# Performance work log

Hardware: AMD Instinct MI355X
Metric: run time of the kernel (lower is better)

Reference implementation:

```python
import jax, jax.numpy as jnp
import numpy as np

D_MODEL = 1024
N_EXPERTS = 8
TOP_K = 2
BOTTLENECK = 64
B, S = 2, 4096
ADAPTER_SCALE = 0.5


def setup_inputs() -> dict:
    key = jax.random.key(0)
    ks = jax.random.split(key, 8)
    sd = 0.02
    x = jax.random.normal(ks[0], (B, S, D_MODEL), dtype=jnp.float32)
    w_gate = jax.random.normal(ks[1], (D_MODEL, N_EXPERTS), dtype=jnp.float32) * sd
    w_noise = jax.random.normal(ks[2], (D_MODEL, N_EXPERTS), dtype=jnp.float32) * sd
    Wd = jax.random.normal(ks[3], (N_EXPERTS, D_MODEL, BOTTLENECK), dtype=jnp.float32) * sd
    bd = jnp.zeros((N_EXPERTS, BOTTLENECK), dtype=jnp.float32)
    Wu = jax.random.normal(ks[4], (N_EXPERTS, BOTTLENECK, D_MODEL), dtype=jnp.float32) * sd
    bu = jnp.zeros((N_EXPERTS, D_MODEL), dtype=jnp.float32)
    return {"x": x, "w_gate": w_gate, "w_noise": w_noise,
            "Wd": Wd, "bd": bd, "Wu": Wu, "bu": bu}


def _moe_forward(x, w_gate, w_noise, Wd, bd, Wu, bu):
    b, s, d = x.shape
    xf = x.reshape(-1, d)                      # [T, D] flattened tokens
    T = xf.shape[0]

    # --- noisy top-k gating (eval mode: no noise added, logits = clean) ---
    clean_logits = xf @ w_gate                 # [T, E]
    logits = clean_logits
    k1 = min(TOP_K + 1, N_EXPERTS)
    top_logits, top_idx = jax.lax.top_k(logits, k1)
    top_k_logits = top_logits[:, :TOP_K]       # [T, k]
    top_k_idx = top_idx[:, :TOP_K]             # [T, k]
    top_k_gates = jax.nn.softmax(top_k_logits, axis=-1)
    rows = jnp.arange(T)[:, None]
    gates = jnp.zeros((T, N_EXPERTS), dtype=top_k_gates.dtype)
    gates = gates.at[rows, top_k_idx].set(top_k_gates)  # sparse gate matrix [T, E]

    # --- experts (AdaptFormer adapters): dense compute, sparse combine ---
    # mathematically identical to SparseDispatcher dispatch/combine:
    # out[t] = sum_e gates[t,e] * expert_e(x[t])  (gates zero off top-k)
    h = jax.nn.relu(jnp.einsum('td,edb->teb', xf, Wd) + bd[None, :, :])  # [T,E,b]
    y = jnp.einsum('teb,ebd->ted', h, Wu) + bu[None, :, :]               # [T,E,D]
    y = ADAPTER_SCALE * y
    out = jnp.einsum('te,ted->td', gates, y)   # weighted combine (index_add equiv)
    return out.reshape(b, s, d)


def reference(x, w_gate, w_noise, Wd, bd, Wu, bu):
    return _moe_forward(x, w_gate, w_noise, Wd, bd, Wu, bu)
```

## Files before the change

kernel.cpp:

```cpp
#include <hip/hip_runtime.h>
#include <stdint.h>

#define T_TOK 8192
#define DM    1024
#define NE    8
#define BOT   64
#define HD    512
#define HD2   576
#define PW    8

typedef __attribute__((ext_vector_type(8))) short bf16x8;
typedef __attribute__((ext_vector_type(4))) short bf16x4;
typedef __attribute__((ext_vector_type(4))) float f32x4;

__device__ __forceinline__ ushort f2bf(float f) {
  union { float f; uint32_t u; } v; v.f = f;
  uint32_t r = (v.u + 0x7fffu + ((v.u >> 16) & 1u)) >> 16;
  return (ushort)r;
}

__global__ __launch_bounds__(256, 2)
void prep_kernel(const float* __restrict__ x, const float* __restrict__ wg,
                 ushort* __restrict__ Xb, float* __restrict__ sg,
                 ushort* __restrict__ H2) {
  __shared__ float part[4][PW][NE];
  __shared__ float sgl[PW][NE];
  const int lane = threadIdx.x & 63;
  const int w    = threadIdx.x >> 6;
  const int t0   = blockIdx.x * PW;
  const int dd   = w * 256 + lane * 4;

  float4 wgr[4][2];
  #pragma unroll
  for (int j = 0; j < 4; ++j) {
    wgr[j][0] = *(const float4*)(wg + (size_t)(dd + j) * NE);
    wgr[j][1] = *(const float4*)(wg + (size_t)(dd + j) * NE + 4);
  }
  const int ebit = ((lane & 1) << 2) | (lane & 2) | ((lane >> 2) & 1);

  const float* xp = x + (size_t)t0 * DM + dd;
  float4 xv = *(const float4*)xp;
  #pragma unroll
  for (int tk = 0; tk < PW; ++tk) {
    float4 nxt = {};
    if (tk + 1 < PW) nxt = *(const float4*)(xp + (size_t)(tk + 1) * DM);
    bf16x4 xb;
    xb[0] = (short)f2bf(xv.x); xb[1] = (short)f2bf(xv.y);
    xb[2] = (short)f2bf(xv.z); xb[3] = (short)f2bf(xv.w);
    *(bf16x4*)(Xb + (size_t)(t0 + tk) * DM + dd) = xb;
    float a[NE] = {};
    const float* xs = (const float*)&xv;
    #pragma unroll
    for (int j = 0; j < 4; ++j) {
      const float xj = xs[j];
      const float* wr = (const float*)&wgr[j][0];
      #pragma unroll
      for (int e = 0; e < NE; ++e) a[e] += xj * wr[e];
    }
    float t0v[4];
    #pragma unroll
    for (int j = 0; j < 4; ++j) {
      float send = (lane & 1) ? a[j] : a[j + 4];
      float keep = (lane & 1) ? a[j + 4] : a[j];
      t0v[j] = keep + __shfl_xor(send, 1);
    }
    float t1v[2];
    #pragma unroll
    for (int j = 0; j < 2; ++j) {
      float send = (lane & 2) ? t0v[j] : t0v[j + 2];
      float keep = (lane & 2) ? t0v[j + 2] : t0v[j];
      t1v[j] = keep + __shfl_xor(send, 2);
    }
    {
      float send = (lane & 4) ? t1v[0] : t1v[1];
      float keep = (lane & 4) ? t1v[1] : t1v[0];
      float t2 = keep + __shfl_xor(send, 4);
      t2 += __shfl_xor(t2, 8);
      t2 += __shfl_xor(t2, 16);
      t2 += __shfl_xor(t2, 32);
      if (lane < NE) part[w][tk][ebit] = t2;
    }
    xv = nxt;
  }
  __syncthreads();

  const int tid = threadIdx.x;
  if (tid < PW) {
    float lg[NE];
    #pragma unroll
    for (int e = 0; e < NE; ++e)
      lg[e] = part[0][tid][e] + part[1][tid][e] + part[2][tid][e] + part[3][tid][e];
    int e0 = 0; float l0 = lg[0];
    #pragma unroll
    for (int e = 1; e < NE; ++e) if (lg[e] > l0) { l0 = lg[e]; e0 = e; }
    int e1 = -1; float l1 = -3.4e38f;
    #pragma unroll
    for (int e = 0; e < NE; ++e) if (e != e0 && lg[e] > l1) { l1 = lg[e]; e1 = e; }
    const float p1  = __expf(l1 - l0);
    const float inv = 1.f / (1.f + p1);
    const float g0 = 0.5f * inv, g1 = 0.5f * p1 * inv;
    float g[NE];
    #pragma unroll
    for (int e = 0; e < NE; ++e) g[e] = (e == e0) ? g0 : ((e == e1) ? g1 : 0.f);
    #pragma unroll
    for (int e = 0; e < NE; ++e) sgl[tid][e] = g[e];
    *(float4*)(sg + (size_t)(t0 + tid) * NE)     = *(float4*)&g[0];
    *(float4*)(sg + (size_t)(t0 + tid) * NE + 4) = *(float4*)&g[4];
  }
  __syncthreads();

  if (tid < PW * 8) {
    const int tk = tid >> 3, ch = tid & 7;
    bf16x8 v;
    #pragma unroll
    for (int k = 0; k < 8; ++k)
      v[k] = (ch == 0) ? (short)f2bf(sgl[tk][k]) : (short)0;
    *(bf16x8*)(H2 + (size_t)(t0 + tk) * HD2 + HD + ch * 8) = v;
  }
}

__global__ __launch_bounds__(256)
void cvt_w_kernel(const float* __restrict__ Wd, const float* __restrict__ Wu,
                  const float* __restrict__ bu,
                  ushort* __restrict__ WdT, ushort* __restrict__ Wu2T) {
  __shared__ ushort tl[64][72];
  const int rr = threadIdx.x >> 2;
  const int cc = (threadIdx.x & 3) * 16;
  const int bx = blockIdx.x;
  if (bx < 128) {
    const int e  = bx >> 4;
    const int d0 = (bx & 15) * 64;
    const float* src = Wd + ((size_t)e * DM + d0 + rr) * BOT + cc;
    #pragma unroll
    for (int i = 0; i < 4; ++i) {
      float4 v = *(const float4*)(src + i * 4);
      tl[rr][cc + i * 4 + 0] = f2bf(v.x);
      tl[rr][cc + i * 4 + 1] = f2bf(v.y);
      tl[rr][cc + i * 4 + 2] = f2bf(v.z);
      tl[rr][cc + i * 4 + 3] = f2bf(v.w);
    }
    __syncthreads();
    bf16x8 o0, o1;
    #pragma unroll
    for (int k = 0; k < 8; ++k) o0[k] = (short)tl[cc + k][rr];
    #pragma unroll
    for (int k = 0; k < 8; ++k) o1[k] = (short)tl[cc + 8 + k][rr];
    ushort* dst = WdT + ((size_t)e * BOT + rr) * DM + d0 + cc;
    *(bf16x8*)dst       = o0;
    *(bf16x8*)(dst + 8) = o1;
  } else {
    const int b2 = bx - 128;
    const int n0 = (b2 >> 4) * 64;
    const int d0 = (b2 & 15) * 64;
    const int n  = n0 + rr;
    #pragma unroll
    for (int i = 0; i < 4; ++i) {
      float4 v;
      if (n < HD)           v = *(const float4*)(Wu + (size_t)n * DM + d0 + cc + i * 4);
      else if (n < HD + NE) v = *(const float4*)(bu + (size_t)(n - HD) * DM + d0 + cc + i * 4);
      else { v.x = 0.f; v.y = 0.f; v.z = 0.f; v.w = 0.f; }
      tl[rr][cc + i * 4 + 0] = f2bf(v.x);
      tl[rr][cc + i * 4 + 1] = f2bf(v.y);
      tl[rr][cc + i * 4 + 2] = f2bf(v.z);
      tl[rr][cc + i * 4 + 3] = f2bf(v.w);
    }
    __syncthreads();
    bf16x8 o0, o1;
    #pragma unroll
    for (int k = 0; k < 8; ++k) o0[k] = (short)tl[cc + k][rr];
    #pragma unroll
    for (int k = 0; k < 8; ++k) o1[k] = (short)tl[cc + 8 + k][rr];
    ushort* dst = Wu2T + (size_t)(d0 + rr) * HD2 + n0 + cc;
    *(bf16x8*)dst       = o0;
    *(bf16x8*)(dst + 8) = o1;
  }
}

template <int EPI, int NKT, int NBX>
__global__ __launch_bounds__(256)
void gemm_bt(const ushort* __restrict__ A, const ushort* __restrict__ B,
             const float* __restrict__ sg, const float* __restrict__ bd,
             ushort* __restrict__ Hout, float* __restrict__ Cout, int nwg) {
  constexpr int K = NKT * 64;
  __shared__ __attribute__((aligned(16))) ushort sA[2][128 * 64];
  __shared__ __attribute__((aligned(16))) ushort sB[2][128 * 64];
  const int lane = threadIdx.x & 63;
  const int w    = threadIdx.x >> 6;
  const int lb = (blockIdx.x % 8) * (nwg / 8) + blockIdx.x / 8;
  const int tile_m = (lb / NBX) * 128;
  const int tile_n = (lb % NBX) * 128;
  const int wm = (w >> 1) * 64;
  const int wn = (w & 1) * 64;
  const int sr = lane >> 3;
  const int sc = ((lane & 7) * 8) ^ (sr << 3);
  const int lr = lane & 15;
  const int kg = lane >> 4;
  const int swz = (lr & 7) << 3;
  f32x4 acc[4][4] = {};

#define STAGE(buf, kt) do {                                                       \
    const int k0_ = (kt) << 6;                                                    \
    _Pragma("unroll")                                                             \
    for (int c = 0; c < 4; ++c) {                                                 \
      const ushort* ga = A + (size_t)(tile_m + w * 32 + c * 8 + sr) * K + k0_ + sc; \
      __builtin_amdgcn_global_load_lds((const __attribute__((address_space(1))) void*)ga, \
          (__attribute__((address_space(3))) void*)&sA[buf][(w * 32 + c * 8) * 64], 16, 0, 0); \
      const ushort* gb = B + (size_t)(tile_n + w * 32 + c * 8 + sr) * K + k0_ + sc; \
      __builtin_amdgcn_global_load_lds((const __attribute__((address_space(1))) void*)gb, \
          (__attribute__((address_space(3))) void*)&sB[buf][(w * 32 + c * 8) * 64], 16, 0, 0); \
    } } while (0)

  STAGE(0, 0);
  for (int kt = 0; kt < NKT; ++kt) {
    const int cur = kt & 1;
    if (kt + 1 < NKT) {
      STAGE(cur ^ 1, kt + 1);
      asm volatile("s_waitcnt vmcnt(8)" ::: "memory");
    } else {
      asm volatile("s_waitcnt vmcnt(0)" ::: "memory");
    }
    __builtin_amdgcn_s_barrier();
    #pragma unroll
    for (int s = 0; s < 2; ++s) {
      bf16x8 af[4], bfr[4];
      #pragma unroll
      for (int i = 0; i < 4; ++i)
        af[i] = *(const bf16x8*)&sA[cur][(wm + i * 16 + lr) * 64 + ((s * 32 + kg * 8) ^ swz)];
      #pragma unroll
      for (int j = 0; j < 4; ++j)
        bfr[j] = *(const bf16x8*)&sB[cur][(wn + j * 16 + lr) * 64 + ((s * 32 + kg * 8) ^ swz)];
      #pragma unroll
      for (int i = 0; i < 4; ++i)
        #pragma unroll
        for (int j = 0; j < 4; ++j)
          acc[i][j] = __builtin_amdgcn_mfma_f32_16x16x32_bf16(af[i], bfr[j], acc[i][j], 0, 0, 0);
    }
    asm volatile("" ::: "memory");
    __builtin_amdgcn_s_barrier();
  }
#undef STAGE

  if (EPI == 0) {
    const int e = (tile_n + wn) >> 6;
    float bdv[4];
    #pragma unroll
    for (int j = 0; j < 4; ++j) bdv[j] = bd[tile_n + wn + j * 16 + lr];
    #pragma unroll
    for (int i = 0; i < 4; ++i) {
      #pragma unroll
      for (int r = 0; r < 4; ++r) {
        const int t = tile_m + wm + i * 16 + kg * 4 + r;
        const float sglv = sg[(size_t)t * NE + e];
        #pragma unroll
        for (int j = 0; j < 4; ++j) {
          float v = fmaxf(acc[i][j][r] + bdv[j], 0.f) * sglv;
          Hout[(size_t)t * HD2 + tile_n + wn + j * 16 + lr] = f2bf(v);
        }
      }
    }
  } else {
    #pragma unroll
    for (int i = 0; i < 4; ++i) {
      #pragma unroll
      for (int r = 0; r < 4; ++r) {
        const int t = tile_m + wm + i * 16 + kg * 4 + r;
        #pragma unroll
        for (int j = 0; j < 4; ++j)
          Cout[(size_t)t * DM + tile_n + wn + j * 16 + lr] = acc[i][j][r];
      }
    }
  }
}

extern "C" void kernel_launch(void* const* d_in, const int* in_sizes, int n_in,
                              void* d_out, int out_size, void* d_ws, size_t ws_size,
                              hipStream_t stream) {
  const float* x  = (const float*)d_in[0];
  const float* wg = (const float*)d_in[1];
  const float* Wd = (const float*)d_in[3];
  const float* bd = (const float*)d_in[4];
  const float* Wu = (const float*)d_in[5];
  const float* bu = (const float*)d_in[6];
  float* out = (float*)d_out;

  char* ws = (char*)d_ws;
  ushort* Xb   = (ushort*)(ws);
  ushort* H2   = (ushort*)(ws + 16777216);
  ushort* WdT  = (ushort*)(ws + 26214400);
  ushort* Wu2T = (ushort*)(ws + 27262976);
  float*  sgw  = (float*) (ws + 28442624);

  prep_kernel <<<dim3(T_TOK / PW), dim3(256), 0, stream>>>(x, wg, Xb, sgw, H2);
  cvt_w_kernel<<<dim3(272),        dim3(256), 0, stream>>>(Wd, Wu, bu, WdT, Wu2T);

  gemm_bt<0, 16, 4><<<dim3(256), dim3(256), 0, stream>>>(Xb, WdT, sgw, bd, H2, nullptr, 256);
  gemm_bt<1, 9, 8><<<dim3(512), dim3(256), 0, stream>>>(H2, Wu2T, sgw, nullptr, nullptr, out, 512);
}
```

Before: 55.54 us.

## Merge prep and weight-convert kernels, use 128x64 GEMM tiles with triple buffering

Merges the token prep/gating kernel and the weight conversion kernel into a single launch, with blocks selected by block index, to save one launch and let the two jobs overlap. The GEMM tile shrinks from 128x128 to 128x64, doubling the grid to 512 and 1024 workgroups for better CU coverage. The shared-memory pipeline goes from double to triple buffering with two tiles prefetched ahead, waitcnts adjusted to match. Smaller N tiles reload more of A per output and lower MFMA work per LDS read.

After: 50.38 us. 1.1x faster.

```diff
diff --git a/kernel.cpp b/kernel.cpp
--- a/kernel.cpp
+++ b/kernel.cpp
@@ -8,6 +8,7 @@
 #define HD    512
 #define HD2   576
 #define PW    8
+#define NPREP (T_TOK / PW)
 
 typedef __attribute__((ext_vector_type(8))) short bf16x8;
 typedef __attribute__((ext_vector_type(4))) short bf16x4;
@@ -20,159 +21,155 @@
 }
 
 __global__ __launch_bounds__(256, 2)
-void prep_kernel(const float* __restrict__ x, const float* __restrict__ wg,
-                 ushort* __restrict__ Xb, float* __restrict__ sg,
-                 ushort* __restrict__ H2) {
+void prep_cvt_kernel(const float* __restrict__ x, const float* __restrict__ wg,
+                     const float* __restrict__ Wd, const float* __restrict__ Wu,
+                     const float* __restrict__ bu,
+                     ushort* __restrict__ Xb, float* __restrict__ sg,
+                     ushort* __restrict__ H2, ushort* __restrict__ WdT,
+                     ushort* __restrict__ Wu2T) {
   __shared__ float part[4][PW][NE];
   __shared__ float sgl[PW][NE];
-  const int lane = threadIdx.x & 63;
-  const int w    = threadIdx.x >> 6;
-  const int t0   = blockIdx.x * PW;
-  const int dd   = w * 256 + lane * 4;
-
-  float4 wgr[4][2];
-  #pragma unroll
-  for (int j = 0; j < 4; ++j) {
-    wgr[j][0] = *(const float4*)(wg + (size_t)(dd + j) * NE);
-    wgr[j][1] = *(const float4*)(wg + (size_t)(dd + j) * NE + 4);
-  }
-  const int ebit = ((lane & 1) << 2) | (lane & 2) | ((lane >> 2) & 1);
-
-  const float* xp = x + (size_t)t0 * DM + dd;
-  float4 xv = *(const float4*)xp;
-  #pragma unroll
-  for (int tk = 0; tk < PW; ++tk) {
-    float4 nxt = {};
-    if (tk + 1 < PW) nxt = *(const float4*)(xp + (size_t)(tk + 1) * DM);
-    bf16x4 xb;
-    xb[0] = (short)f2bf(xv.x); xb[1] = (short)f2bf(xv.y);
-    xb[2] = (short)f2bf(xv.z); xb[3] = (short)f2bf(xv.w);
-    *(bf16x4*)(Xb + (size_t)(t0 + tk) * DM + dd) = xb;
-    float a[NE] = {};
-    const float* xs = (const float*)&xv;
+  __shared__ ushort tl[64][72];
+  if (blockIdx.x < NPREP) {
+    const int lane = threadIdx.x & 63;
+    const int w    = threadIdx.x >> 6;
+    const int t0   = blockIdx.x * PW;
+    const int dd   = w * 256 + lane * 4;
+    float4 wgr[4][2];
     #pragma unroll
     for (int j = 0; j < 4; ++j) {
-      const float xj = xs[j];
-      const float* wr = (const float*)&wgr[j][0];
-      #pragma unroll
-      for (int e = 0; e < NE; ++e) a[e] += xj * wr[e];
-    }
-    float t0v[4];
-    #pragma unroll
-    for (int j = 0; j < 4; ++j) {
-      float send = (lane & 1) ? a[j] : a[j + 4];
-      float keep = (lane & 1) ? a[j + 4] : a[j];
-      t0v[j] = keep + __shfl_xor(send, 1);
-    }
-    float t1v[2];
-    #pragma unroll
-    for (int j = 0; j < 2; ++j) {
-      float send = (lane & 2) ? t0v[j] : t0v[j + 2];
-      float keep = (lane & 2) ? t0v[j + 2] : t0v[j];
-      t1v[j] = keep + __shfl_xor(send, 2);
-    }
-    {
-      float send = (lane & 4) ? t1v[0] : t1v[1];
-      float keep = (lane & 4) ? t1v[1] : t1v[0];
-      float t2 = keep + __shfl_xor(send, 4);
-      t2 += __shfl_xor(t2, 8);
-      t2 += __shfl_xor(t2, 16);
-      t2 += __shfl_xor(t2, 32);
-      if (lane < NE) part[w][tk][ebit] = t2;
-    }
-    xv = nxt;
-  }
-  __syncthreads();
-
-  const int tid = threadIdx.x;
-  if (tid < PW) {
-    float lg[NE];
-    #pragma unroll
-    for (int e = 0; e < NE; ++e)
-      lg[e] = part[0][tid][e] + part[1][tid][e] + part[2][tid][e] + part[3][tid][e];
-    int e0 = 0; float l0 = lg[0];
-    #pragma unroll
-    for (int e = 1; e < NE; ++e) if (lg[e] > l0) { l0 = lg[e]; e0 = e; }
-    int e1 = -1; float l1 = -3.4e38f;
-    #pragma unroll
-    for (int e = 0; e < NE; ++e) if (e != e0 && lg[e] > l1) { l1 = lg[e]; e1 = e; }
-    const float p1  = __expf(l1 - l0);
-    const float inv = 1.f / (1.f + p1);
-    const float g0 = 0.5f * inv, g1 = 0.5f * p1 * inv;
-    float g[NE];
-    #pragma unroll
-    for (int e = 0; e < NE; ++e) g[e] = (e == e0) ? g0 : ((e == e1) ? g1 : 0.f);
-    #pragma unroll
-    for (int e = 0; e < NE; ++e) sgl[tid][e] = g[e];
-    *(float4*)(sg + (size_t)(t0 + tid) * NE)     = *(float4*)&g[0];
-    *(float4*)(sg + (size_t)(t0 + tid) * NE + 4) = *(float4*)&g[4];
-  }
-  __syncthreads();
-
-  if (tid < PW * 8) {
-    const int tk = tid >> 3, ch = tid & 7;
-    bf16x8 v;
-    #pragma unroll
-    for (int k = 0; k < 8; ++k)
-      v[k] = (ch == 0) ? (short)f2bf(sgl[tk][k]) : (short)0;
-    *(bf16x8*)(H2 + (size_t)(t0 + tk) * HD2 + HD + ch * 8) = v;
-  }
-}
-
-__global__ __launch_bounds__(256)
-void cvt_w_kernel(const float* __restrict__ Wd, const float* __restrict__ Wu,
-                  const float* __restrict__ bu,
-                  ushort* __restrict__ WdT, ushort* __restrict__ Wu2T) {
-  __shared__ ushort tl[64][72];
-  const int rr = threadIdx.x >> 2;
-  const int cc = (threadIdx.x & 3) * 16;
-  const int bx = blockIdx.x;
-  if (bx < 128) {
-    const int e  = bx >> 4;
-    const int d0 = (bx & 15) * 64;
-    const float* src = Wd + ((size_t)e * DM + d0 + rr) * BOT + cc;
-    #pragma unroll
-    for (int i = 0; i < 4; ++i) {
-      float4 v = *(const float4*)(src + i * 4);
-      tl[rr][cc + i * 4 + 0] = f2bf(v.x);
-      tl[rr][cc + i * 4 + 1] = f2bf(v.y);
-      tl[rr][cc + i * 4 + 2] = f2bf(v.z);
-      tl[rr][cc + i * 4 + 3] = f2bf(v.w);
+      wgr[j][0] = *(const float4*)(wg + (size_t)(dd + j) * NE);
+      wgr[j][1] = *(const float4*)(wg + (size_t)(dd + j) * NE + 4);
+    }
+    const int ebit = ((lane & 1) << 2) | (lane & 2) | ((lane >> 2) & 1);
+    const float* xp = x + (size_t)t0 * DM + dd;
+    float4 xv = *(const float4*)xp;
+    #pragma unroll
+    for (int tk = 0; tk < PW; ++tk) {
+      float4 nxt = {};
+      if (tk + 1 < PW) nxt = *(const float4*)(xp + (size_t)(tk + 1) * DM);
+      bf16x4 xb;
+      xb[0] = (short)f2bf(xv.x); xb[1] = (short)f2bf(xv.y);
+      xb[2] = (short)f2bf(xv.z); xb[3] = (short)f2bf(xv.w);
+      *(bf16x4*)(Xb + (size_t)(t0 + tk) * DM + dd) = xb;
+      float a[NE] = {};
+      const float* xs = (const float*)&xv;
+      #pragma unroll
+      for (int j = 0; j < 4; ++j) {
+        const float xj = xs[j];
+        const float* wr = (const float*)&wgr[j][0];
+        #pragma unroll
+        for (int e = 0; e < NE; ++e) a[e] += xj * wr[e];
+      }
+      float t0v[4];
+      #pragma unroll
+      for (int j = 0; j < 4; ++j) {
+        float send = (lane & 1) ? a[j] : a[j + 4];
+        float keep = (lane & 1) ? a[j + 4] : a[j];
+        t0v[j] = keep + __shfl_xor(send, 1);
+      }
+      float t1v[2];
+      #pragma unroll
+      for (int j = 0; j < 2; ++j) {
+        float send = (lane & 2) ? t0v[j] : t0v[j + 2];
+        float keep = (lane & 2) ? t0v[j + 2] : t0v[j];
+        t1v[j] = keep + __shfl_xor(send, 2);
+      }
+      {
+        float send = (lane & 4) ? t1v[0] : t1v[1];
+        float keep = (lane & 4) ? t1v[1] : t1v[0];
+        float t2 = keep + __shfl_xor(send, 4);
+        t2 += __shfl_xor(t2, 8);
+        t2 += __shfl_xor(t2, 16);
+        t2 += __shfl_xor(t2, 32);
+        if (lane < NE) part[w][tk][ebit] = t2;
+      }
+      xv = nxt;
     }
     __syncthreads();
-    bf16x8 o0, o1;
-    #pragma unroll
-    for (int k = 0; k < 8; ++k) o0[k] = (short)tl[cc + k][rr];
-    #pragma unroll
-    for (int k = 0; k < 8; ++k) o1[k] = (short)tl[cc + 8 + k][rr];
-    ushort* dst = WdT + ((size_t)e * BOT + rr) * DM + d0 + cc;
-    *(bf16x8*)dst       = o0;
-    *(bf16x8*)(dst + 8) = o1;
+    const int tid = threadIdx.x;
+    if (tid < PW) {
+      float lg[NE];
+      #pragma unroll
+      for (int e = 0; e < NE; ++e)
+        lg[e] = part[0][tid][e] + part[1][tid][e] + part[2][tid][e] + part[3][tid][e];
+      int e0 = 0; float l0 = lg[0];
+      #pragma unroll
+      for (int e = 1; e < NE; ++e) if (lg[e] > l0) { l0 = lg[e]; e0 = e; }
+      int e1 = -1; float l1 = -3.4e38f;
+      #pragma unroll
+      for (int e = 0; e < NE; ++e) if (e != e0 && lg[e] > l1) { l1 = lg[e]; e1 = e; }
+      const float p1  = __expf(l1 - l0);
+      const float inv = 1.f / (1.f + p1);
+      const float g0 = 0.5f * inv, g1 = 0.5f * p1 * inv;
+      float g[NE];
+      #pragma unroll
+      for (int e = 0; e < NE; ++e) g[e] = (e == e0) ? g0 : ((e == e1) ? g1 : 0.f);
+      #pragma unroll
+      for (int e = 0; e < NE; ++e) sgl[tid][e] = g[e];
+      *(float4*)(sg + (size_t)(t0 + tid) * NE)     = *(float4*)&g[0];
+      *(float4*)(sg + (size_t)(t0 + tid) * NE + 4) = *(float4*)&g[4];
+    }
+    __syncthreads();
+    if (tid < PW * 8) {
+      const int tk = tid >> 3, ch = tid & 7;
+      bf16x8 v;
+      #pragma unroll
+      for (int k = 0; k < 8; ++k)
+        v[k] = (ch == 0) ? (short)f2bf(sgl[tk][k]) : (short)0;
+      *(bf16x8*)(H2 + (size_t)(t0 + tk) * HD2 + HD + ch * 8) = v;
+    }
   } else {
-    const int b2 = bx - 128;
-    const int n0 = (b2 >> 4) * 64;
-    const int d0 = (b2 & 15) * 64;
-    const int n  = n0 + rr;
-    #pragma unroll
-    for (int i = 0; i < 4; ++i) {
-      float4 v;
-      if (n < HD)           v = *(const float4*)(Wu + (size_t)n * DM + d0 + cc + i * 4);
-      else if (n < HD + NE) v = *(const float4*)(bu + (size_t)(n - HD) * DM + d0 + cc + i * 4);
-      else { v.x = 0.f; v.y = 0.f; v.z = 0.f; v.w = 0.f; }
-      tl[rr][cc + i * 4 + 0] = f2bf(v.x);
-      tl[rr][cc + i * 4 + 1] = f2bf(v.y);
-      tl[rr][cc + i * 4 + 2] = f2bf(v.z);
-      tl[rr][cc + i * 4 + 3] = f2bf(v.w);
-    }
-    __syncthreads();
-    bf16x8 o0, o1;
-    #pragma unroll
-    for (int k = 0; k < 8; ++k) o0[k] = (short)tl[cc + k][rr];
-    #pragma unroll
-    for (int k = 0; k < 8; ++k) o1[k] = (short)tl[cc + 8 + k][rr];
-    ushort* dst = Wu2T + (size_t)(d0 + rr) * HD2 + n0 + cc;
-    *(bf16x8*)dst       = o0;
-    *(bf16x8*)(dst + 8) = o1;
+    const int rr = threadIdx.x >> 2;
+    const int cc = (threadIdx.x & 3) * 16;
+    const int bx = blockIdx.x - NPREP;
+    if (bx < 128) {
+      const int e  = bx >> 4;
+      const int d0 = (bx & 15) * 64;
+      const float* src = Wd + ((size_t)e * DM + d0 + rr) * BOT + cc;
+      #pragma unroll
+      for (int i = 0; i < 4; ++i) {
+        float4 v = *(const float4*)(src + i * 4);
+        tl[rr][cc + i * 4 + 0] = f2bf(v.x);
+        tl[rr][cc + i * 4 + 1] = f2bf(v.y);
+        tl[rr][cc + i * 4 + 2] = f2bf(v.z);
+        tl[rr][cc + i * 4 + 3] = f2bf(v.w);
+      }
+      __syncthreads();
+      bf16x8 o0, o1;
+      #pragma unroll
+      for (int k = 0; k < 8; ++k) o0[k] = (short)tl[cc + k][rr];
+      #pragma unroll
+      for (int k = 0; k < 8; ++k) o1[k] = (short)tl[cc + 8 + k][rr];
+      ushort* dst = WdT + ((size_t)e * BOT + rr) * DM + d0 + cc;
+      *(bf16x8*)dst       = o0;
+      *(bf16x8*)(dst + 8) = o1;
+    } else {
+      const int b2 = bx - 128;
+      const int n0 = (b2 >> 4) * 64;
+      const int d0 = (b2 & 15) * 64;
+      const int n  = n0 + rr;
+      #pragma unroll
+      for (int i = 0; i < 4; ++i) {
+        float4 v;
+        if (n < HD)           v = *(const float4*)(Wu + (size_t)n * DM + d0 + cc + i * 4);
+        else if (n < HD + NE) v = *(const float4*)(bu + (size_t)(n - HD) * DM + d0 + cc + i * 4);
+        else { v.x = 0.f; v.y = 0.f; v.z = 0.f; v.w = 0.f; }
+        tl[rr][cc + i * 4 + 0] = f2bf(v.x);
+        tl[rr][cc + i * 4 + 1] = f2bf(v.y);
+        tl[rr][cc + i * 4 + 2] = f2bf(v.z);
+        tl[rr][cc + i * 4 + 3] = f2bf(v.w);
+      }
+      __syncthreads();
+      bf16x8 o0, o1;
+      #pragma unroll
+      for (int k = 0; k < 8; ++k) o0[k] = (short)tl[cc + k][rr];
+      #pragma unroll
+      for (int k = 0; k < 8; ++k) o1[k] = (short)tl[cc + 8 + k][rr];
+      ushort* dst = Wu2T + (size_t)(d0 + rr) * HD2 + n0 + cc;
+      *(bf16x8*)dst       = o0;
+      *(bf16x8*)(dst + 8) = o1;
+    }
   }
 }
 
@@ -182,21 +179,21 @@
              const float* __restrict__ sg, const float* __restrict__ bd,
              ushort* __restrict__ Hout, float* __restrict__ Cout, int nwg) {
   constexpr int K = NKT * 64;
-  __shared__ __attribute__((aligned(16))) ushort sA[2][128 * 64];
-  __shared__ __attribute__((aligned(16))) ushort sB[2][128 * 64];
+  __shared__ __attribute__((aligned(16))) ushort sA[3][128 * 64];
+  __shared__ __attribute__((aligned(16))) ushort sB[3][64 * 64];
   const int lane = threadIdx.x & 63;
   const int w    = threadIdx.x >> 6;
   const int lb = (blockIdx.x % 8) * (nwg / 8) + blockIdx.x / 8;
   const int tile_m = (lb / NBX) * 128;
-  const int tile_n = (lb % NBX) * 128;
+  const int tile_n = (lb % NBX) * 64;
   const int wm = (w >> 1) * 64;
-  const int wn = (w & 1) * 64;
+  const int wn = (w & 1) * 32;
   const int sr = lane >> 3;
   const int sc = ((lane & 7) * 8) ^ (sr << 3);
   const int lr = lane & 15;
   const int kg = lane >> 4;
   const int swz = (lr & 7) << 3;
-  f32x4 acc[4][4] = {};
+  f32x4 acc[4][2] = {};
 
 #define STAGE(buf, kt) do {                                                       \
     const int k0_ = (kt) << 6;                                                    \
@@ -205,34 +202,40 @@
       const ushort* ga = A + (size_t)(tile_m + w * 32 + c * 8 + sr) * K + k0_ + sc; \
       __builtin_amdgcn_global_load_lds((const __attribute__((address_space(1))) void*)ga, \
           (__attribute__((address_space(3))) void*)&sA[buf][(w * 32 + c * 8) * 64], 16, 0, 0); \
-      const ushort* gb = B + (size_t)(tile_n + w * 32 + c * 8 + sr) * K + k0_ + sc; \
+    }                                                                             \
+    _Pragma("unroll")                                                             \
+    for (int c = 0; c < 2; ++c) {                                                 \
+      const ushort* gb = B + (size_t)(tile_n + w * 16 + c * 8 + sr) * K + k0_ + sc; \
       __builtin_amdgcn_global_load_lds((const __attribute__((address_space(1))) void*)gb, \
-          (__attribute__((address_space(3))) void*)&sB[buf][(w * 32 + c * 8) * 64], 16, 0, 0); \
+          (__attribute__((address_space(3))) void*)&sB[buf][(w * 16 + c * 8) * 64], 16, 0, 0); \
     } } while (0)
 
   STAGE(0, 0);
+  STAGE(1, 1);
   for (int kt = 0; kt < NKT; ++kt) {
-    const int cur = kt & 1;
-    if (kt + 1 < NKT) {
-      STAGE(cur ^ 1, kt + 1);
-      asm volatile("s_waitcnt vmcnt(8)" ::: "memory");
+    const int cur = kt % 3;
+    if (kt + 2 < NKT) {
+      STAGE((kt + 2) % 3, kt + 2);
+      asm volatile("s_waitcnt vmcnt(12)" ::: "memory");
+    } else if (kt + 1 < NKT) {
+      asm volatile("s_waitcnt vmcnt(6)" ::: "memory");
     } else {
       asm volatile("s_waitcnt vmcnt(0)" ::: "memory");
     }
     __builtin_amdgcn_s_barrier();
     #pragma unroll
     for (int s = 0; s < 2; ++s) {
-      bf16x8 af[4], bfr[4];
+      bf16x8 af[4], bfr[2];
       #pragma unroll
       for (int i = 0; i < 4; ++i)
         af[i] = *(const bf16x8*)&sA[cur][(wm + i * 16 + lr) * 64 + ((s * 32 + kg * 8) ^ swz)];
       #pragma unroll
-      for (int j = 0; j < 4; ++j)
+      for (int j = 0; j < 2; ++j)
         bfr[j] = *(const bf16x8*)&sB[cur][(wn + j * 16 + lr) * 64 + ((s * 32 + kg * 8) ^ swz)];
       #pragma unroll
       for (int i = 0; i < 4; ++i)
         #pragma unroll
-        for (int j = 0; j < 4; ++j)
+        for (int j = 0; j < 2; ++j)
           acc[i][j] = __builtin_amdgcn_mfma_f32_16x16x32_bf16(af[i], bfr[j], acc[i][j], 0, 0, 0);
     }
     asm volatile("" ::: "memory");
@@ -241,10 +244,10 @@
 #undef STAGE
 
   if (EPI == 0) {
-    const int e = (tile_n + wn) >> 6;
-    float bdv[4];
-    #pragma unroll
-    for (int j = 0; j < 4; ++j) bdv[j] = bd[tile_n + wn + j * 16 + lr];
+    const int e = tile_n >> 6;
+    float bdv[2];
+    #pragma unroll
+    for (int j = 0; j < 2; ++j) bdv[j] = bd[tile_n + wn + j * 16 + lr];
     #pragma unroll
     for (int i = 0; i < 4; ++i) {
       #pragma unroll
@@ -252,7 +255,7 @@
         const int t = tile_m + wm + i * 16 + kg * 4 + r;
         const float sglv = sg[(size_t)t * NE + e];
         #pragma unroll
-        for (int j = 0; j < 4; ++j) {
+        for (int j = 0; j < 2; ++j) {
           float v = fmaxf(acc[i][j][r] + bdv[j], 0.f) * sglv;
           Hout[(size_t)t * HD2 + tile_n + wn + j * 16 + lr] = f2bf(v);
         }
@@ -265,7 +268,7 @@
       for (int r = 0; r < 4; ++r) {
         const int t = tile_m + wm + i * 16 + kg * 4 + r;
         #pragma unroll
-        for (int j = 0; j < 4; ++j)
+        for (int j = 0; j < 2; ++j)
           Cout[(size_t)t * DM + tile_n + wn + j * 16 + lr] = acc[i][j][r];
       }
     }
@@ -290,9 +293,9 @@
   ushort* Wu2T = (ushort*)(ws + 27262976);
   float*  sgw  = (float*) (ws + 28442624);
 
-  prep_kernel <<<dim3(T_TOK / PW), dim3(256), 0, stream>>>(x, wg, Xb, sgw, H2);
-  cvt_w_kernel<<<dim3(272),        dim3(256), 0, stream>>>(Wd, Wu, bu, WdT, Wu2T);
-
-  gemm_bt<0, 16, 4><<<dim3(256), dim3(256), 0, stream>>>(Xb, WdT, sgw, bd, H2, nullptr, 256);
-  gemm_bt<1, 9, 8><<<dim3(512), dim3(256), 0, stream>>>(H2, Wu2T, sgw, nullptr, nullptr, out, 512);
+  prep_cvt_kernel<<<dim3(NPREP + 272), dim3(256), 0, stream>>>(
+      x, wg, Wd, Wu, bu, Xb, sgw, H2, WdT, Wu2T);
+
+  gemm_bt<0, 16, 8><<<dim3(512), dim3(256), 0, stream>>>(Xb, WdT, sgw, bd, H2, nullptr, 512);
+  gemm_bt<1, 9, 16><<<dim3(1024), dim3(256), 0, stream>>>(H2, Wu2T, sgw, nullptr, nullptr, out, 1024);
 }
```

## Merge prep and weight-convert kernels; use 256-row tiles in up-projection GEMM

Applied to the files above, without the earlier changes.

Folds the activation-prep/gating kernel and the weight-convert kernel into one launch, using block-index ranges to pick the role. This removes one kernel launch and the gap between the two. The GEMM is templated on the M tile size. The up-projection GEMM now uses 256x128 tiles with 512 threads, which halves the number of workgroups and increases reuse of the B tile. Load distribution across waves and the vmcnt wait count are adjusted to match. MFMA sections are wrapped in s_setprio to favour math issue, at the risk of register pressure under the 512-thread launch bound.

Measured after the change: 52.94 us. 4.7% less time.

```diff
diff --git a/kernel.cpp b/kernel.cpp
--- a/kernel.cpp
+++ b/kernel.cpp
@@ -8,6 +8,7 @@
 #define HD    512
 #define HD2   576
 #define PW    8
+#define NPREP (T_TOK / PW)
 
 typedef __attribute__((ext_vector_type(8))) short bf16x8;
 typedef __attribute__((ext_vector_type(4))) short bf16x4;
@@ -20,174 +21,174 @@
 }
 
 __global__ __launch_bounds__(256, 2)
-void prep_kernel(const float* __restrict__ x, const float* __restrict__ wg,
-                 ushort* __restrict__ Xb, float* __restrict__ sg,
-                 ushort* __restrict__ H2) {
+void prep_cvt_kernel(const float* __restrict__ x, const float* __restrict__ wg,
+                     const float* __restrict__ Wd, const float* __restrict__ Wu,
+                     const float* __restrict__ bu,
+                     ushort* __restrict__ Xb, float* __restrict__ sg,
+                     ushort* __restrict__ H2, ushort* __restrict__ WdT,
+                     ushort* __restrict__ Wu2T) {
   __shared__ float part[4][PW][NE];
   __shared__ float sgl[PW][NE];
-  const int lane = threadIdx.x & 63;
-  const int w    = threadIdx.x >> 6;
-  const int t0   = blockIdx.x * PW;
-  const int dd   = w * 256 + lane * 4;
-
-  float4 wgr[4][2];
-  #pragma unroll
-  for (int j = 0; j < 4; ++j) {
-    wgr[j][0] = *(const float4*)(wg + (size_t)(dd + j) * NE);
-    wgr[j][1] = *(const float4*)(wg + (size_t)(dd + j) * NE + 4);
-  }
-  const int ebit = ((lane & 1) << 2) | (lane & 2) | ((lane >> 2) & 1);
-
-  const float* xp = x + (size_t)t0 * DM + dd;
-  float4 xv = *(const float4*)xp;
-  #pragma unroll
-  for (int tk = 0; tk < PW; ++tk) {
-    float4 nxt = {};
-    if (tk + 1 < PW) nxt = *(const float4*)(xp + (size_t)(tk + 1) * DM);
-    bf16x4 xb;
-    xb[0] = (short)f2bf(xv.x); xb[1] = (short)f2bf(xv.y);
-    xb[2] = (short)f2bf(xv.z); xb[3] = (short)f2bf(xv.w);
-    *(bf16x4*)(Xb + (size_t)(t0 + tk) * DM + dd) = xb;
-    float a[NE] = {};
-    const float* xs = (const float*)&xv;
+  __shared__ ushort tl[64][72];
+  if (blockIdx.x < NPREP) {
+    const int lane = threadIdx.x & 63;
+    const int w    = threadIdx.x >> 6;
+    const int t0   = blockIdx.x * PW;
+    const int dd   = w * 256 + lane * 4;
+    float4 wgr[4][2];
     #pragma unroll
     for (int j = 0; j < 4; ++j) {
-      const float xj = xs[j];
-      const float* wr = (const float*)&wgr[j][0];
-      #pragma unroll
-      for (int e = 0; e < NE; ++e) a[e] += xj * wr[e];
-    }
-    float t0v[4];
-    #pragma unroll
-    for (int j = 0; j < 4; ++j) {
-      float send = (lane & 1) ? a[j] : a[j + 4];
-      float keep = (lane & 1) ? a[j + 4] : a[j];
-      t0v[j] = keep + __shfl_xor(send, 1);
-    }
-    float t1v[2];
-    #pragma unroll
-    for (int j = 0; j < 2; ++j) {
-      float send = (lane & 2) ? t0v[j] : t0v[j + 2];
-      float keep = (lane & 2) ? t0v[j + 2] : t0v[j];
-      t1v[j] = keep + __shfl_xor(send, 2);
-    }
-    {
-      float send = (lane & 4) ? t1v[0] : t1v[1];
-      float keep = (lane & 4) ? t1v[1] : t1v[0];
-      float t2 = keep + __shfl_xor(send, 4);
-      t2 += __shfl_xor(t2, 8);
-      t2 += __shfl_xor(t2, 16);
-      t2 += __shfl_xor(t2, 32);
-      if (lane < NE) part[w][tk][ebit] = t2;
-    }
-    xv = nxt;
-  }
-  __syncthreads();
-
-  const int tid = threadIdx.x;
-  if (tid < PW) {
-    float lg[NE];
-    #pragma unroll
-    for (int e = 0; e < NE; ++e)
-      lg[e] = part[0][tid][e] + part[1][tid][e] + part[2][tid][e] + part[3][tid][e];
-    int e0 = 0; float l0 = lg[0];
-    #pragma unroll
-    for (int e = 1; e < NE; ++e) if (lg[e] > l0) { l0 = lg[e]; e0 = e; }
-    int e1 = -1; float l1 = -3.4e38f;
-    #pragma unroll
-    for (int e = 0; e < NE; ++e) if (e != e0 && lg[e] > l1) { l1 = lg[e]; e1 = e; }
-    const float p1  = __expf(l1 - l0);
-    const float inv = 1.f / (1.f + p1);
-    const float g0 = 0.5f * inv, g1 = 0.5f * p1 * inv;
-    float g[NE];
-    #pragma unroll
-    for (int e = 0; e < NE; ++e) g[e] = (e == e0) ? g0 : ((e == e1) ? g1 : 0.f);
-    #pragma unroll
-    for (int e = 0; e < NE; ++e) sgl[tid][e] = g[e];
-    *(float4*)(sg + (size_t)(t0 + tid) * NE)     = *(float4*)&g[0];
-    *(float4*)(sg + (size_t)(t0 + tid) * NE + 4) = *(float4*)&g[4];
-  }
-  __syncthreads();
-
-  if (tid < PW * 8) {
-    const int tk = tid >> 3, ch = tid & 7;
-    bf16x8 v;
-    #pragma unroll
-    for (int k = 0; k < 8; ++k)
-      v[k] = (ch == 0) ? (short)f2bf(sgl[tk][k]) : (short)0;
-    *(bf16x8*)(H2 + (size_t)(t0 + tk) * HD2 + HD + ch * 8) = v;
+      wgr[j][0] = *(const float4*)(wg + (size_t)(dd + j) * NE);
+      wgr[j][1] = *(const float4*)(wg + (size_t)(dd + j) * NE + 4);
+    }
+    const int ebit = ((lane & 1) << 2) | (lane & 2) | ((lane >> 2) & 1);
+    const float* xp = x + (size_t)t0 * DM + dd;
+    float4 xv = *(const float4*)xp;
+    #pragma unroll
+    for (int tk = 0; tk < PW; ++tk) {
+      float4 nxt = {};
+      if (tk + 1 < PW) nxt = *(const float4*)(xp + (size_t)(tk + 1) * DM);
+      bf16x4 xb;
+      xb[0] = (short)f2bf(xv.x); xb[1] = (short)f2bf(xv.y);
+      xb[2] = (short)f2bf(xv.z); xb[3] = (short)f2bf(xv.w);
+      *(bf16x4*)(Xb + (size_t)(t0 + tk) * DM + dd) = xb;
+      float a[NE] = {};
+      const float* xs = (const float*)&xv;
+      #pragma unroll
+      for (int j = 0; j < 4; ++j) {
+        const float xj = xs[j];
+        const float* wr = (const float*)&wgr[j][0];
+        #pragma unroll
+        for (int e = 0; e < NE; ++e) a[e] += xj * wr[e];
+      }
+      float t0v[4];
+      #pragma unroll
+      for (int j = 0; j < 4; ++j) {
+        float send = (lane & 1) ? a[j] : a[j + 4];
+        float keep = (lane & 1) ? a[j + 4] : a[j];
+        t0v[j] = keep + __shfl_xor(send, 1);
+      }
+      float t1v[2];
+      #pragma unroll
+      for (int j = 0; j < 2; ++j) {
+        float send = (lane & 2) ? t0v[j] : t0v[j + 2];
+        float keep = (lane & 2) ? t0v[j + 2] : t0v[j];
+        t1v[j] = keep + __shfl_xor(send, 2);
+      }
+      {
+        float send = (lane & 4) ? t1v[0] : t1v[1];
+        float keep = (lane & 4) ? t1v[1] : t1v[0];
+        float t2 = keep + __shfl_xor(send, 4);
+        t2 += __shfl_xor(t2, 8);
+        t2 += __shfl_xor(t2, 16);
+        t2 += __shfl_xor(t2, 32);
+        if (lane < NE) part[w][tk][ebit] = t2;
+      }
+      xv = nxt;
+    }
+    __syncthreads();
+    const int tid = threadIdx.x;
+    if (tid < PW) {
+      float lg[NE];
+      #pragma unroll
+      for (int e = 0; e < NE; ++e)
+        lg[e] = part[0][tid][e] + part[1][tid][e] + part[2][tid][e] + part[3][tid][e];
+      int e0 = 0; float l0 = lg[0];
+      #pragma unroll
+      for (int e = 1; e < NE; ++e) if (lg[e] > l0) { l0 = lg[e]; e0 = e; }
+      int e1 = -1; float l1 = -3.4e38f;
+      #pragma unroll
+      for (int e = 0; e < NE; ++e) if (e != e0 && lg[e] > l1) { l1 = lg[e]; e1 = e; }
+      const float p1  = __expf(l1 - l0);
+      const float inv = 1.f / (1.f + p1);
+      const float g0 = 0.5f * inv, g1 = 0.5f * p1 * inv;
+      float g[NE];
+      #pragma unroll
+      for (int e = 0; e < NE; ++e) g[e] = (e == e0) ? g0 : ((e == e1) ? g1 : 0.f);
+      #pragma unroll
+      for (int e = 0; e < NE; ++e) sgl[tid][e] = g[e];
+      *(float4*)(sg + (size_t)(t0 + tid) * NE)     = *(float4*)&g[0];
+      *(float4*)(sg + (size_t)(t0 + tid) * NE + 4) = *(float4*)&g[4];
+    }
+    __syncthreads();
+    if (tid < PW * 8) {
+      const int tk = tid >> 3, ch = tid & 7;
+      bf16x8 v;
+      #pragma unroll
+      for (int k = 0; k < 8; ++k)
+        v[k] = (ch == 0) ? (short)f2bf(sgl[tk][k]) : (short)0;
+      *(bf16x8*)(H2 + (size_t)(t0 + tk) * HD2 + HD + ch * 8) = v;
+    }
+  } else {
+    const int rr = threadIdx.x >> 2;
+    const int cc = (threadIdx.x & 3) * 16;
+    const int bx = blockIdx.x - NPREP;
+    if (bx < 128) {
+      const int e  = bx >> 4;
+      const int d0 = (bx & 15) * 64;
+      const float* src = Wd + ((size_t)e * DM + d0 + rr) * BOT + cc;
+      #pragma unroll
+      for (int i = 0; i < 4; ++i) {
+        float4 v = *(const float4*)(src + i * 4);
+        tl[rr][cc + i * 4 + 0] = f2bf(v.x);
+        tl[rr][cc + i * 4 + 1] = f2bf(v.y);
+        tl[rr][cc + i * 4 + 2] = f2bf(v.z);
+        tl[rr][cc + i * 4 + 3] = f2bf(v.w);
+      }
+      __syncthreads();
+      bf16x8 o0, o1;
+      #pragma unroll
+      for (int k = 0; k < 8; ++k) o0[k] = (short)tl[cc + k][rr];
+      #pragma unroll
+      for (int k = 0; k < 8; ++k) o1[k] = (short)tl[cc + 8 + k][rr];
+      ushort* dst = WdT + ((size_t)e * BOT + rr) * DM + d0 + cc;
+      *(bf16x8*)dst       = o0;
+      *(bf16x8*)(dst + 8) = o1;
+    } else {
+      const int b2 = bx - 128;
+      const int n0 = (b2 >> 4) * 64;
+      const int d0 = (b2 & 15) * 64;
+      const int n  = n0 + rr;
+      #pragma unroll
+      for (int i = 0; i < 4; ++i) {
+        float4 v;
+        if (n < HD)           v = *(const float4*)(Wu + (size_t)n * DM + d0 + cc + i * 4);
+        else if (n < HD + NE) v = *(const float4*)(bu + (size_t)(n - HD) * DM + d0 + cc + i * 4);
+        else { v.x = 0.f; v.y = 0.f; v.z = 0.f; v.w = 0.f; }
+        tl[rr][cc + i * 4 + 0] = f2bf(v.x);
+        tl[rr][cc + i * 4 + 1] = f2bf(v.y);
+        tl[rr][cc + i * 4 + 2] = f2bf(v.z);
+        tl[rr][cc + i * 4 + 3] = f2bf(v.w);
+      }
+      __syncthreads();
+      bf16x8 o0, o1;
+      #pragma unroll
+      for (int k = 0; k < 8; ++k) o0[k] = (short)tl[cc + k][rr];
+      #pragma unroll
+      for (int k = 0; k < 8; ++k) o1[k] = (short)tl[cc + 8 + k][rr];
+      ushort* dst = Wu2T + (size_t)(d0 + rr) * HD2 + n0 + cc;
+      *(bf16x8*)dst       = o0;
+      *(bf16x8*)(dst + 8) = o1;
+    }
   }
 }
 
-__global__ __launch_bounds__(256)
-void cvt_w_kernel(const float* __restrict__ Wd, const float* __restrict__ Wu,
-                  const float* __restrict__ bu,
-                  ushort* __restrict__ WdT, ushort* __restrict__ Wu2T) {
-  __shared__ ushort tl[64][72];
-  const int rr = threadIdx.x >> 2;
-  const int cc = (threadIdx.x & 3) * 16;
-  const int bx = blockIdx.x;
-  if (bx < 128) {
-    const int e  = bx >> 4;
-    const int d0 = (bx & 15) * 64;
-    const float* src = Wd + ((size_t)e * DM + d0 + rr) * BOT + cc;
-    #pragma unroll
-    for (int i = 0; i < 4; ++i) {
-      float4 v = *(const float4*)(src + i * 4);
-      tl[rr][cc + i * 4 + 0] = f2bf(v.x);
-      tl[rr][cc + i * 4 + 1] = f2bf(v.y);
-      tl[rr][cc + i * 4 + 2] = f2bf(v.z);
-      tl[rr][cc + i * 4 + 3] = f2bf(v.w);
-    }
-    __syncthreads();
-    bf16x8 o0, o1;
-    #pragma unroll
-    for (int k = 0; k < 8; ++k) o0[k] = (short)tl[cc + k][rr];
-    #pragma unroll
-    for (int k = 0; k < 8; ++k) o1[k] = (short)tl[cc + 8 + k][rr];
-    ushort* dst = WdT + ((size_t)e * BOT + rr) * DM + d0 + cc;
-    *(bf16x8*)dst       = o0;
-    *(bf16x8*)(dst + 8) = o1;
-  } else {
-    const int b2 = bx - 128;
-    const int n0 = (b2 >> 4) * 64;
-    const int d0 = (b2 & 15) * 64;
-    const int n  = n0 + rr;
-    #pragma unroll
-    for (int i = 0; i < 4; ++i) {
-      float4 v;
-      if (n < HD)           v = *(const float4*)(Wu + (size_t)n * DM + d0 + cc + i * 4);
-      else if (n < HD + NE) v = *(const float4*)(bu + (size_t)(n - HD) * DM + d0 + cc + i * 4);
-      else { v.x = 0.f; v.y = 0.f; v.z = 0.f; v.w = 0.f; }
-      tl[rr][cc + i * 4 + 0] = f2bf(v.x);
-      tl[rr][cc + i * 4 + 1] = f2bf(v.y);
-      tl[rr][cc + i * 4 + 2] = f2bf(v.z);
-      tl[rr][cc + i * 4 + 3] = f2bf(v.w);
-    }
-    __syncthreads();
-    bf16x8 o0, o1;
-    #pragma unroll
-    for (int k = 0; k < 8; ++k) o0[k] = (short)tl[cc + k][rr];
-    #pragma unroll
-    for (int k = 0; k < 8; ++k) o1[k] = (short)tl[cc + 8 + k][rr];
-    ushort* dst = Wu2T + (size_t)(d0 + rr) * HD2 + n0 + cc;
-    *(bf16x8*)dst       = o0;
-    *(bf16x8*)(dst + 8) = o1;
-  }
-}
-
-template <int EPI, int NKT, int NBX>
-__global__ __launch_bounds__(256)
+template <int EPI, int NKT, int NBX, int BM>
+__global__ __launch_bounds__(BM * 2, 2)
 void gemm_bt(const ushort* __restrict__ A, const ushort* __restrict__ B,
              const float* __restrict__ sg, const float* __restrict__ bd,
              ushort* __restrict__ Hout, float* __restrict__ Cout, int nwg) {
-  constexpr int K = NKT * 64;
-  __shared__ __attribute__((aligned(16))) ushort sA[2][128 * 64];
+  constexpr int K   = NKT * 64;
+  constexpr int NW  = BM / 32;
+  constexpr int AU  = BM / 8;
+  constexpr int TU  = AU + 16;
+  constexpr int UPW = TU / NW;
+  __shared__ __attribute__((aligned(16))) ushort sA[2][BM * 64];
   __shared__ __attribute__((aligned(16))) ushort sB[2][128 * 64];
   const int lane = threadIdx.x & 63;
   const int w    = threadIdx.x >> 6;
   const int lb = (blockIdx.x % 8) * (nwg / 8) + blockIdx.x / 8;
-  const int tile_m = (lb / NBX) * 128;
+  const int tile_m = (lb / NBX) * BM;
   const int tile_n = (lb % NBX) * 128;
   const int wm = (w >> 1) * 64;
   const int wn = (w & 1) * 64;
@@ -198,16 +199,20 @@
   const int swz = (lr & 7) << 3;
   f32x4 acc[4][4] = {};
 
-#define STAGE(buf, kt) do {                                                       \
-    const int k0_ = (kt) << 6;                                                    \
-    _Pragma("unroll")                                                             \
-    for (int c = 0; c < 4; ++c) {                                                 \
-      const ushort* ga = A + (size_t)(tile_m + w * 32 + c * 8 + sr) * K + k0_ + sc; \
-      __builtin_amdgcn_global_load_lds((const __attribute__((address_space(1))) void*)ga, \
-          (__attribute__((address_space(3))) void*)&sA[buf][(w * 32 + c * 8) * 64], 16, 0, 0); \
-      const ushort* gb = B + (size_t)(tile_n + w * 32 + c * 8 + sr) * K + k0_ + sc; \
-      __builtin_amdgcn_global_load_lds((const __attribute__((address_space(1))) void*)gb, \
-          (__attribute__((address_space(3))) void*)&sB[buf][(w * 32 + c * 8) * 64], 16, 0, 0); \
+#define STAGE(buf, kt) do {                                                         \
+    const int k0_ = (kt) << 6;                                                      \
+    _Pragma("unroll")                                                               \
+    for (int c = 0; c < UPW; ++c) {                                                 \
+      const int u = w * UPW + c;                                                    \
+      if (u < AU) {                                                                 \
+        const ushort* ga = A + (size_t)(tile_m + u * 8 + sr) * K + k0_ + sc;        \
+        __builtin_amdgcn_global_load_lds((const __attribute__((address_space(1))) void*)ga, \
+            (__attribute__((address_space(3))) void*)&sA[buf][u * 512], 16, 0, 0);  \
+      } else {                                                                      \
+        const ushort* gb = B + (size_t)(tile_n + (u - AU) * 8 + sr) * K + k0_ + sc; \
+        __builtin_amdgcn_global_load_lds((const __attribute__((address_space(1))) void*)gb, \
+            (__attribute__((address_space(3))) void*)&sB[buf][(u - AU) * 512], 16, 0, 0); \
+      }                                                                             \
     } } while (0)
 
   STAGE(0, 0);
@@ -215,7 +220,8 @@
     const int cur = kt & 1;
     if (kt + 1 < NKT) {
       STAGE(cur ^ 1, kt + 1);
-      asm volatile("s_waitcnt vmcnt(8)" ::: "memory");
+      if (UPW == 8) asm volatile("s_waitcnt vmcnt(8)" ::: "memory");
+      else          asm volatile("s_waitcnt vmcnt(6)" ::: "memory");
     } else {
       asm volatile("s_waitcnt vmcnt(0)" ::: "memory");
     }
@@ -229,11 +235,13 @@
       #pragma unroll
       for (int j = 0; j < 4; ++j)
         bfr[j] = *(const bf16x8*)&sB[cur][(wn + j * 16 + lr) * 64 + ((s * 32 + kg * 8) ^ swz)];
+      __builtin_amdgcn_s_setprio(1);
       #pragma unroll
       for (int i = 0; i < 4; ++i)
         #pragma unroll
         for (int j = 0; j < 4; ++j)
           acc[i][j] = __builtin_amdgcn_mfma_f32_16x16x32_bf16(af[i], bfr[j], acc[i][j], 0, 0, 0);
+      __builtin_amdgcn_s_setprio(0);
     }
     asm volatile("" ::: "memory");
     __builtin_amdgcn_s_barrier();
@@ -290,9 +298,11 @@
   ushort* Wu2T = (ushort*)(ws + 27262976);
   float*  sgw  = (float*) (ws + 28442624);
 
-  prep_kernel <<<dim3(T_TOK / PW), dim3(256), 0, stream>>>(x, wg, Xb, sgw, H2);
-  cvt_w_kernel<<<dim3(272),        dim3(256), 0, stream>>>(Wd, Wu, bu, WdT, Wu2T);
-
-  gemm_bt<0, 16, 4><<<dim3(256), dim3(256), 0, stream>>>(Xb, WdT, sgw, bd, H2, nullptr, 256);
-  gemm_bt<1, 9, 8><<<dim3(512), dim3(256), 0, stream>>>(H2, Wu2T, sgw, nullptr, nullptr, out, 512);
+  prep_cvt_kernel<<<dim3(NPREP + 272), dim3(256), 0, stream>>>(
+      x, wg, Wd, Wu, bu, Xb, sgw, H2, WdT, Wu2T);
+
+  gemm_bt<0, 16, 4, 128><<<dim3(256), dim3(256), 0, stream>>>(
+      Xb, WdT, sgw, bd, H2, nullptr, 256);
+  gemm_bt<1, 9, 8, 256><<<dim3(256), dim3(512), 0, stream>>>(
+      H2, Wu2T, sgw, nullptr, nullptr, out, 256);
 }
```
